# Performance work log

Measured on AMD Instinct MI355X. Metric: run time of the kernel, lower is better.

The kernel has to match this reference:

```python
import jax, jax.numpy as jnp
import numpy as np

B, T, I, H, O = 32, 128, 256, 512, 10


def setup_inputs() -> dict:
    key = jax.random.key(0)
    ks = jax.random.split(key, 16)
    s = 1.0 / np.sqrt(H)
    si = 1.0 / np.sqrt(I)
    inp = {
        "x": jax.random.normal(ks[0], (B, T, I), jnp.float32),
        # LSTM params (gate order: i, f, g, o)
        "Wih": jax.random.uniform(ks[1], (4 * H, I), jnp.float32, -si, si),
        "Whh": jax.random.uniform(ks[2], (4 * H, H), jnp.float32, -s, s),
        "b_lstm": jax.random.uniform(ks[3], (4 * H,), jnp.float32, -s, s),
        # readout dense
        "Wd": jax.random.uniform(ks[4], (O, H), jnp.float32, -s, s),
        "bd": jnp.zeros((O,), jnp.float32),
        # synthetic gradient MLP: H -> 512 -> 256 -> 128 -> H
        "Ws1": jax.random.uniform(ks[5], (512, H), jnp.float32, -s, s),
        "bs1": jnp.zeros((512,), jnp.float32),
        "Ws2": jax.random.uniform(ks[6], (256, 512), jnp.float32, -1.0 / np.sqrt(512), 1.0 / np.sqrt(512)),
        "bs2": jnp.zeros((256,), jnp.float32),
        "Ws3": jax.random.uniform(ks[7], (128, 256), jnp.float32, -1.0 / np.sqrt(256), 1.0 / np.sqrt(256)),
        "bs3": jnp.zeros((128,), jnp.float32),
        "Ws4": jax.random.uniform(ks[8], (H, 128), jnp.float32, -1.0 / np.sqrt(128), 1.0 / np.sqrt(128)),
        "bs4": jnp.zeros((H,), jnp.float32),
    }
    return inp


def reference(x, Wih, Whh, b_lstm, Wd, bd, Ws1, bs1, Ws2, bs2, Ws3, bs3, Ws4, bs4):
    # batch_first: [B,T,I] -> [T,B,I]
    xs = jnp.swapaxes(x, 0, 1)
    b, hid = x.shape[0], Whh.shape[1]

    h0 = jnp.zeros((b, hid), x.dtype)
    c0 = jnp.zeros((b, hid), x.dtype)
    # e-prop eligibility vectors: one row per (gate in {i,f,g}) x hidden unit
    ev_x0 = jnp.zeros((b, 3 * hid, Wih.shape[1]), x.dtype)
    ev_h0 = jnp.zeros((b, 3 * hid, hid), x.dtype)
    ev_b0 = jnp.zeros((b, 3 * hid, 1), x.dtype)

    def step(carry, xt):
        h, c, ev_x, ev_h, ev_b = carry
        gates = xt @ Wih.T + h @ Whh.T + b_lstm  # [B,4H]
        gi, gf, gg, go = jnp.split(gates, 4, axis=1)
        i = jax.nn.sigmoid(gi)
        f = jax.nn.sigmoid(gf)
        g = jnp.tanh(gg)
        o = jax.nn.sigmoid(go)
        # d(c_t)/d(pre-activation) for cell-affecting gates i, f, g  -> [B,3H]
        d = jnp.concatenate([g * i * (1.0 - i),
                             c * f * (1.0 - f),
                             i * (1.0 - g * g)], axis=1)
        f3 = jnp.concatenate([f, f, f], axis=1)  # forget-gate decay, tiled per gate
        # eligibility trace outer-product updates (the memory-bound core)
        ev_x_n = ev_x * f3[:, :, None] + d[:, :, None] * xt[:, None, :]
        ev_h_n = ev_h * f3[:, :, None] + d[:, :, None] * h[:, None, :]
        ev_b_n = ev_b * f3[:, :, None] + d[:, :, None]
        c_n = f * c + i * g
        h_n = o * jnp.tanh(c_n)
        return (h_n, c_n, ev_x_n, ev_h_n, ev_b_n), h_n

    (hT, cT, ev_x, ev_h, ev_b), hs = jax.lax.scan(step, (h0, c0, ev_x0, ev_h0, ev_b0), xs)

    last = hs[-1]  # [B,H]
    # synthetic gradient MLP on last hidden state
    z = jax.nn.relu(last @ Ws1.T + bs1)
    z = jax.nn.relu(z @ Ws2.T + bs2)
    z = jax.nn.relu(z @ Ws3.T + bs3)
    synth_grad = z @ Ws4.T + bs4  # [B,H]
    # readout on last hidden state (single_output=True)
    predictions = last @ Wd.T + bd  # [B,O]
    return (predictions, synth_grad, ev_x, ev_h, ev_b)
```

## Files before the change

kernel.cpp:

```cpp
#include <hip/hip_runtime.h>


typedef __attribute__((ext_vector_type(8))) short short8;
typedef __attribute__((ext_vector_type(4))) float f32x4;
typedef __attribute__((ext_vector_type(4))) unsigned u32x4;

#define DEV static __device__ __forceinline__

DEV unsigned f2bf(float x) {
  union { float f; unsigned u; } v; v.f = x;
  return (v.u + 0x7fffu + ((v.u >> 16) & 1u)) >> 16;
}
DEV float bf2f(unsigned b) {
  union { float f; unsigned u; } v; v.u = b << 16;
  return v.f;
}
struct HiLo { unsigned hi, lo; };
DEV HiLo packpair(float a, float b) {
  unsigned ha = f2bf(a), hb = f2bf(b);
  unsigned la = f2bf(a - bf2f(ha)), lb = f2bf(b - bf2f(hb));
  HiLo r; r.hi = ha | (hb << 16); r.lo = la | (lb << 16);
  return r;
}

__global__ __launch_bounds__(512, 1) void lstm_rec(
    const float* __restrict__ Whh,
    const float* __restrict__ XW,
    unsigned* __restrict__ Hp,
    float* __restrict__ Hf,
    float* __restrict__ dh,
    float* __restrict__ fh,
    unsigned* __restrict__ flags)
{
  const int wg   = blockIdx.x;
  const int tid  = threadIdx.x;
  const int lane = tid & 63;
  const int wave = tid >> 6;
  const int tM   = wave & 1;
  const int tN   = wave >> 1;

  __shared__ __align__(16) unsigned Ldh[32 * 256];
  __shared__ __align__(16) unsigned Ldl[32 * 256];
  __shared__ float gl[32][68];

  const int cc = lane & 15;
  const int kb = lane >> 4;

  const int rloc  = tN * 16 + cc;
  const int jglob = (rloc >> 4) * 512 + wg * 16 + (rloc & 15);
  short8 whi[16], wlo[16];
#pragma unroll
  for (int s = 0; s < 16; ++s) {
    const float* wp = Whh + (size_t)jglob * 512 + s * 32 + kb * 8;
    f32x4 w0 = *(const f32x4*)wp;
    f32x4 w1 = *(const f32x4*)(wp + 4);
    short8 hi, lo;
#pragma unroll
    for (int j = 0; j < 4; ++j) {
      unsigned h0 = f2bf(w0[j]);
      hi[j] = (short)h0;  lo[j] = (short)f2bf(w0[j] - bf2f(h0));
      unsigned h1 = f2bf(w1[j]);
      hi[4 + j] = (short)h1;  lo[4 + j] = (short)f2bf(w1[j] - bf2f(h1));
    }
    whi[s] = hi; wlo[s] = lo;
  }

  const int bA = tM * 16 + cc;
  const int mz = bA & 7;
  const unsigned rbase = (unsigned)(bA * 256 + ((kb ^ (mz & 3)) << 2) + ((mz >> 2) << 4));

  const int beW = lane >> 1;
  const int swz = beW & 7;

  const int be = tid >> 4;
  const int jo = tid & 15;
  const int jh = wg * 16 + jo;
  float c_reg = 0.f;

  for (int t = 0; t < 128; ++t) {
    const float* xwp = XW + (size_t)t * 65536 + (size_t)be * 2048 + wg * 16 + jo;
    float xwi = xwp[0], xwf = xwp[512], xwg = xwp[1024], xwo = xwp[1536];

    if (t > 0) {
      const unsigned long long* fl =
          (const unsigned long long*)(flags + t * 32 + wave * 4);
      for (;;) {
        unsigned long long f0 = __hip_atomic_load(fl, __ATOMIC_RELAXED,
                                                  __HIP_MEMORY_SCOPE_AGENT);
        unsigned long long f1 = __hip_atomic_load(fl + 1, __ATOMIC_RELAXED,
                                                  __HIP_MEMORY_SCOPE_AGENT);
        unsigned long long v = f0 & f1;
        if (v & (v >> 32) & 1ull) break;
        __builtin_amdgcn_s_sleep(1);
      }

      const unsigned* sp = Hp + ((size_t)t * 32 + wave * 4) * 512 + lane * 4;
      u32x4 h0, l0, h1, l1, h2, l2, h3, l3;
#define SLICE_LOAD(dst, addr)                                          \
      asm volatile("global_load_dwordx4 %0, %1, off sc0 sc1"           \
                   : "=&v"(dst) : "v"(addr) : "memory")
      SLICE_LOAD(h0, sp);
      SLICE_LOAD(l0, sp + 256);
      SLICE_LOAD(h1, sp + 512);
      SLICE_LOAD(l1, sp + 768);
      SLICE_LOAD(h2, sp + 1024);
      SLICE_LOAD(l2, sp + 1280);
      SLICE_LOAD(h3, sp + 1536);
      SLICE_LOAD(l3, sp + 1792);
#undef SLICE_LOAD
      asm volatile("s_waitcnt vmcnt(0)" ::: "memory");
      __builtin_amdgcn_sched_barrier(0);

      const int c0 = wave * 8 + (lane & 1);
      const unsigned wb = (unsigned)(beW * 256);
      *(u32x4*)&Ldh[wb + (((c0 + 0) ^ swz) << 2)] = h0;
      *(u32x4*)&Ldl[wb + (((c0 + 0) ^ swz) << 2)] = l0;
      *(u32x4*)&Ldh[wb + (((c0 + 2) ^ swz) << 2)] = h1;
      *(u32x4*)&Ldl[wb + (((c0 + 2) ^ swz) << 2)] = l1;
      *(u32x4*)&Ldh[wb + (((c0 + 4) ^ swz) << 2)] = h2;
      *(u32x4*)&Ldl[wb + (((c0 + 4) ^ swz) << 2)] = l2;
      *(u32x4*)&Ldh[wb + (((c0 + 6) ^ swz) << 2)] = h3;
      *(u32x4*)&Ldl[wb + (((c0 + 6) ^ swz) << 2)] = l3;
    }
    __syncthreads();

    f32x4 acc = {0.f, 0.f, 0.f, 0.f};
    if (t > 0) {
#pragma unroll
      for (int s = 0; s < 16; ++s) {
        const unsigned idx = rbase ^ (unsigned)(s << 4);
        short8 ah = __builtin_bit_cast(short8, *(const u32x4*)&Ldh[idx]);
        short8 al = __builtin_bit_cast(short8, *(const u32x4*)&Ldl[idx]);
        acc = __builtin_amdgcn_mfma_f32_16x16x32_bf16(ah, whi[s], acc, 0, 0, 0);
        acc = __builtin_amdgcn_mfma_f32_16x16x32_bf16(ah, wlo[s], acc, 0, 0, 0);
        acc = __builtin_amdgcn_mfma_f32_16x16x32_bf16(al, whi[s], acc, 0, 0, 0);
      }
    }
#pragma unroll
    for (int r = 0; r < 4; ++r)
      gl[tM * 16 + kb * 4 + r][tN * 16 + cc] = acc[r];
    __syncthreads();

    {
      float pi = xwi + gl[be][jo];
      float pf = xwf + gl[be][16 + jo];
      float pg = xwg + gl[be][32 + jo];
      float po = xwo + gl[be][48 + jo];
      float ig = 1.f / (1.f + expf(-pi));
      float fg = 1.f / (1.f + expf(-pf));
      float gg = tanhf(pg);
      float og = 1.f / (1.f + expf(-po));
      float di = gg * ig * (1.f - ig);
      float df = c_reg * fg * (1.f - fg);
      float dg = ig * (1.f - gg * gg);
      c_reg = fg * c_reg + ig * gg;
      float hn = og * tanhf(c_reg);
      Hf[(size_t)(t + 1) * 16384 + (size_t)be * 512 + jh] = hn;
      size_t db = (size_t)t * 49152 + (size_t)be * 1536 + jh;
      dh[db] = di; dh[db + 512] = df; dh[db + 1024] = dg;
      fh[(size_t)t * 16384 + (size_t)be * 512 + jh] = fg;

      unsigned hh = f2bf(hn);
      unsigned hl = f2bf(hn - bf2f(hh));
      unsigned hh_nb = (unsigned)__shfl_xor((int)hh, 1);
      unsigned hl_nb = (unsigned)__shfl_xor((int)hl, 1);
      size_t sb = ((size_t)(t + 1) * 32 + wg) * 512;
      unsigned stv; size_t sa;
      if (tid & 1) { stv = hl_nb | (hl << 16); sa = sb + 256 + (tid >> 1); }
      else         { stv = hh | (hh_nb << 16); sa = sb + (tid >> 1); }
      __hip_atomic_store(&Hp[sa], stv, __ATOMIC_RELAXED, __HIP_MEMORY_SCOPE_AGENT);
    }

    asm volatile("s_waitcnt vmcnt(0)" ::: "memory");
    __syncthreads();
    if (tid == 0)
      __hip_atomic_store(&flags[(t + 1) * 32 + wg], 1u,
                         __ATOMIC_RELAXED, __HIP_MEMORY_SCOPE_AGENT);
  }
}

__global__ __launch_bounds__(256) void suffix_pre(
    const float* __restrict__ fh, float* __restrict__ Cp)
{
  const int g = blockIdx.x * 256 + threadIdx.x;
  const int k = g >> 14, bjh = g & 16383;
  const int b = bjh >> 9, jh = bjh & 511;
  float P = 1.f;
  for (int t = k * 32; t < k * 32 + 32; ++t)
    P *= fh[(size_t)t * 16384 + (size_t)b * 512 + jh];
  Cp[g] = P;
}

__global__ __launch_bounds__(256) void suffix_main(
    float* __restrict__ dh, const float* __restrict__ fh,
    const float* __restrict__ Cp, float* __restrict__ Sp)
{
  const int g = blockIdx.x * 256 + threadIdx.x;
  const int k = g >> 14, bjh = g & 16383;
  const int b = bjh >> 9, jh = bjh & 511;
  float F = 1.f;
  for (int k2 = k + 1; k2 < 4; ++k2) F *= Cp[(k2 << 14) | bjh];
  float s0 = 0.f, s1 = 0.f, s2 = 0.f;
  for (int t = k * 32 + 31; t >= k * 32; --t) {
    size_t db = (size_t)t * 49152 + (size_t)b * 1536 + jh;
    float a0 = dh[db] * F, a1 = dh[db + 512] * F, a2 = dh[db + 1024] * F;
    dh[db] = a0; dh[db + 512] = a1; dh[db + 1024] = a2;
    s0 += a0; s1 += a1; s2 += a2;
    F *= fh[(size_t)t * 16384 + (size_t)b * 512 + jh];
  }
  size_t sb = (size_t)(k * 32 + b) * 1536 + jh;
  Sp[sb] = s0; Sp[sb + 512] = s1; Sp[sb + 1024] = s2;
}

__global__ __launch_bounds__(256) void evb_reduce(
    const float* __restrict__ Sp, float* __restrict__ evb)
{
  const int g = blockIdx.x * 256 + threadIdx.x;
  evb[g] = Sp[g] + Sp[49152 + g] + Sp[98304 + g] + Sp[147456 + g];
}

__global__ __launch_bounds__(256, 2) void gemm_bf16s(
    const float* __restrict__ A, const float* __restrict__ B,
    float* __restrict__ C, const float* __restrict__ bias,
    int M, int N, int K,
    long long sAm, long long sAk, long long aBatch,
    long long sBn, long long sBk, long long bBatch,
    long long sCm1, long long sCm2, int M1, long long cBatch)
{
  __shared__ __align__(16) unsigned Ahi[128 * 20], Alo[128 * 20];
  __shared__ __align__(16) unsigned Bhi[128 * 20], Blo[128 * 20];

  const int tid  = threadIdx.x;
  const int lane = tid & 63;
  const int wave = tid >> 6;
  const int wm   = wave >> 1;
  const int wn   = wave & 1;
  const int cc   = lane & 15;
  const int kb   = lane >> 4;
  const long long z = blockIdx.z;
  const float* Ab = A + z * aBatch;
  const float* Bb = B + z * bBatch;
  const int m0 = blockIdx.y * 128, n0 = blockIdx.x * 128;

  f32x4 acc[4][4];
#pragma unroll
  for (int i = 0; i < 4; ++i)
#pragma unroll
    for (int j = 0; j < 4; ++j) acc[i][j] = (f32x4){0.f, 0.f, 0.f, 0.f};

  for (int k0 = 0; k0 < K; k0 += 32) {
    if (sAk == 1) {
      const int r = tid >> 1, half = tid & 1;
      const float* s = Ab + (long long)(m0 + r) * sAm + (k0 + half * 16);
      f32x4 v0 = *(const f32x4*)s;
      f32x4 v1 = *(const f32x4*)(s + 4);
      f32x4 v2 = *(const f32x4*)(s + 8);
      f32x4 v3 = *(const f32x4*)(s + 12);
      u32x4 h0, h1, l0, l1;
      HiLo p;
      p = packpair(v0[0], v0[1]); h0[0] = p.hi; l0[0] = p.lo;
      p = packpair(v0[2], v0[3]); h0[1] = p.hi; l0[1] = p.lo;
      p = packpair(v1[0], v1[1]); h0[2] = p.hi; l0[2] = p.lo;
      p = packpair(v1[2], v1[3]); h0[3] = p.hi; l0[3] = p.lo;
      p = packpair(v2[0], v2[1]); h1[0] = p.hi; l1[0] = p.lo;
      p = packpair(v2[2], v2[3]); h1[1] = p.hi; l1[1] = p.lo;
      p = packpair(v3[0], v3[1]); h1[2] = p.hi; l1[2] = p.lo;
      p = packpair(v3[2], v3[3]); h1[3] = p.hi; l1[3] = p.lo;
      const int o = r * 20 + half * 8;
      *(u32x4*)&Ahi[o] = h0;  *(u32x4*)&Ahi[o + 4] = h1;
      *(u32x4*)&Alo[o] = l0;  *(u32x4*)&Alo[o + 4] = l1;
    } else {
#pragma unroll
      for (int it = 0; it < 2; ++it) {
        const int kp = tid >> 4;
        const int mr = (tid & 15) * 4 + it * 64;
        const float* s0 = Ab + (long long)(k0 + 2 * kp) * sAk + (m0 + mr);
        f32x4 va = *(const f32x4*)s0;
        f32x4 vb = *(const f32x4*)(s0 + sAk);
#pragma unroll
        for (int q = 0; q < 4; ++q) {
          HiLo p = packpair(va[q], vb[q]);
          Ahi[(mr + q) * 20 + kp] = p.hi;
          Alo[(mr + q) * 20 + kp] = p.lo;
        }
      }
    }
    if (sBk == 1) {
      const int r = tid >> 1, half = tid & 1;
      const float* s = Bb + (long long)(n0 + r) * sBn + (k0 + half * 16);
      f32x4 v0 = *(const f32x4*)s;
      f32x4 v1 = *(const f32x4*)(s + 4);
      f32x4 v2 = *(const f32x4*)(s + 8);
      f32x4 v3 = *(const f32x4*)(s + 12);
      u32x4 h0, h1, l0, l1;
      HiLo p;
      p = packpair(v0[0], v0[1]); h0[0] = p.hi; l0[0] = p.lo;
      p = packpair(v0[2], v0[3]); h0[1] = p.hi; l0[1] = p.lo;
      p = packpair(v1[0], v1[1]); h0[2] = p.hi; l0[2] = p.lo;
      p = packpair(v1[2], v1[3]); h0[3] = p.hi; l0[3] = p.lo;
      p = packpair(v2[0], v2[1]); h1[0] = p.hi; l1[0] = p.lo;
      p = packpair(v2[2], v2[3]); h1[1] = p.hi; l1[1] = p.lo;
      p = packpair(v3[0], v3[1]); h1[2] = p.hi; l1[2] = p.lo;
      p = packpair(v3[2], v3[3]); h1[3] = p.hi; l1[3] = p.lo;
      const int o = r * 20 + half * 8;
      *(u32x4*)&Bhi[o] = h0;  *(u32x4*)&Bhi[o + 4] = h1;
      *(u32x4*)&Blo[o] = l0;  *(u32x4*)&Blo[o + 4] = l1;
    } else {
#pragma unroll
      for (int it = 0; it < 2; ++it) {
        const int kp = tid >> 4;
        const int nr = (tid & 15) * 4 + it * 64;
        const float* s0 = Bb + (long long)(k0 + 2 * kp) * sBk + (n0 + nr);
        f32x4 va = *(const f32x4*)s0;
        f32x4 vb = *(const f32x4*)(s0 + sBk);
#pragma unroll
        for (int q = 0; q < 4; ++q) {
          HiLo p = packpair(va[q], vb[q]);
          Bhi[(nr + q) * 20 + kp] = p.hi;
          Blo[(nr + q) * 20 + kp] = p.lo;
        }
      }
    }
    __syncthreads();

    short8 ah[4], al[4], bh[4], bl[4];
#pragma unroll
    for (int mi = 0; mi < 4; ++mi) {
      const int row = wm * 64 + mi * 16 + cc;
      ah[mi] = __builtin_bit_cast(short8, *(const u32x4*)&Ahi[row * 20 + kb * 4]);
      al[mi] = __builtin_bit_cast(short8, *(const u32x4*)&Alo[row * 20 + kb * 4]);
    }
#pragma unroll
    for (int ni = 0; ni < 4; ++ni) {
      const int row = wn * 64 + ni * 16 + cc;
      bh[ni] = __builtin_bit_cast(short8, *(const u32x4*)&Bhi[row * 20 + kb * 4]);
      bl[ni] = __builtin_bit_cast(short8, *(const u32x4*)&Blo[row * 20 + kb * 4]);
    }
#pragma unroll
    for (int mi = 0; mi < 4; ++mi)
#pragma unroll
      for (int ni = 0; ni < 4; ++ni) {
        acc[mi][ni] = __builtin_amdgcn_mfma_f32_16x16x32_bf16(ah[mi], bh[ni], acc[mi][ni], 0, 0, 0);
        acc[mi][ni] = __builtin_amdgcn_mfma_f32_16x16x32_bf16(ah[mi], bl[ni], acc[mi][ni], 0, 0, 0);
        acc[mi][ni] = __builtin_amdgcn_mfma_f32_16x16x32_bf16(al[mi], bh[ni], acc[mi][ni], 0, 0, 0);
      }
    __syncthreads();
  }

#pragma unroll
  for (int ni = 0; ni < 4; ++ni) {
    const int ng = n0 + wn * 64 + ni * 16 + cc;
    const float bv = bias ? bias[ng] : 0.f;
#pragma unroll
    for (int mi = 0; mi < 4; ++mi) {
#pragma unroll
      for (int r = 0; r < 4; ++r) {
        const int mg = m0 + wm * 64 + mi * 16 + kb * 4 + r;
        const long long crow = z * cBatch + (long long)(mg % M1) * sCm1 +
                               (long long)(mg / M1) * sCm2;
        C[crow + ng] = acc[mi][ni][r] + bv;
      }
    }
  }
}

template <int BM, int BN, int TM, int TN>
__global__ __launch_bounds__(256) void gemm_f32(
    const float* __restrict__ A, const float* __restrict__ B,
    float* __restrict__ C, const float* __restrict__ bias,
    int M, int N, int K,
    long long sAm, long long sAk, long long aBatch,
    long long sBn, long long sBk, long long bBatch,
    long long sCm1, long long sCm2, int M1, long long cBatch,
    int relu)
{
  constexpr int BK = 16;
  __shared__ float As[BK][BM + 4];
  __shared__ float Bs[BK][BN + 4];
  const int tid = threadIdx.x;
  const long long z = blockIdx.z;
  const float* Ab = A + z * aBatch;
  const float* Bb = B + z * bBatch;
  const int m0 = blockIdx.y * BM, n0 = blockIdx.x * BN;
  constexpr int tn_cnt = BN / TN;
  const int tm0 = (tid / tn_cnt) * TM;
  const int tn0 = (tid % tn_cnt) * TN;

  float acc[TM][TN];
#pragma unroll
  for (int i = 0; i < TM; ++i)
#pragma unroll
    for (int j = 0; j < TN; ++j) acc[i][j] = 0.f;

  for (int k0 = 0; k0 < K; k0 += BK) {
    if (sAk == 1) {
      for (int m = tid >> 2; m < BM; m += 64) {
        const int kq = (tid & 3) * 4;
        f32x4 v = {0.f, 0.f, 0.f, 0.f};
        if (m0 + m < M) v = *(const f32x4*)(Ab + (long long)(m0 + m) * sAm + (k0 + kq));
        As[kq + 0][m] = v[0]; As[kq + 1][m] = v[1];
        As[kq + 2][m] = v[2]; As[kq + 3][m] = v[3];
      }
    } else {
      constexpr int mq_cnt = BM / 4;
      for (int kk = tid / mq_cnt; kk < BK; kk += 256 / mq_cnt) {
        const int mq = (tid % mq_cnt) * 4;
        f32x4 v = {0.f, 0.f, 0.f, 0.f};
        if (m0 + mq < M) v = *(const f32x4*)(Ab + (long long)(k0 + kk) * sAk + (m0 + mq));
        *(f32x4*)&As[kk][mq] = v;
      }
    }
    if (sBk == 1) {
      for (int n = tid >> 2; n < BN; n += 64) {
        const int kq = (tid & 3) * 4;
        f32x4 v = {0.f, 0.f, 0.f, 0.f};
        if (n0 + n < N) v = *(const f32x4*)(Bb + (long long)(n0 + n) * sBn + (k0 + kq));
        Bs[kq + 0][n] = v[0]; Bs[kq + 1][n] = v[1];
        Bs[kq + 2][n] = v[2]; Bs[kq + 3][n] = v[3];
      }
    } else {
      constexpr int nq_cnt = BN / 4;
      for (int kk = tid / nq_cnt; kk < BK; kk += 256 / nq_cnt) {
        const int nq = (tid % nq_cnt) * 4;
        f32x4 v = {0.f, 0.f, 0.f, 0.f};
        if (n0 + nq < N) v = *(const f32x4*)(Bb + (long long)(k0 + kk) * sBk + (n0 + nq));
        *(f32x4*)&Bs[kk][nq] = v;
      }
    }
    __syncthreads();

#pragma unroll
    for (int kk = 0; kk < BK; ++kk) {
      float a[TM], bb[TN];
#pragma unroll
      for (int i = 0; i < TM; ++i) a[i] = As[kk][tm0 + i];
#pragma unroll
      for (int j = 0; j < TN; ++j) bb[j] = Bs[kk][tn0 + j];
#pragma unroll
      for (int i = 0; i < TM; ++i)
#pragma unroll
        for (int j = 0; j < TN; ++j) acc[i][j] += a[i] * bb[j];
    }
    __syncthreads();
  }

#pragma unroll
  for (int i = 0; i < TM; ++i) {
    const int mg = m0 + tm0 + i;
    if (mg >= M) continue;
    const long long crow = z * cBatch + (long long)(mg % M1) * sCm1 +
                           (long long)(mg / M1) * sCm2;
#pragma unroll
    for (int j = 0; j < TN; ++j) {
      const int ng = n0 + tn0 + j;
      if (ng >= N) continue;
      float v = acc[i][j];
      if (bias) v += bias[ng];
      if (relu) v = fmaxf(v, 0.f);
      C[crow + ng] = v;
    }
  }
}

extern "C" void kernel_launch(void* const* d_in, const int* in_sizes, int n_in,
                              void* d_out, int out_size, void* d_ws, size_t ws_size,
                              hipStream_t stream) {
  const float* x   = (const float*)d_in[0];
  const float* Wih = (const float*)d_in[1];
  const float* Whh = (const float*)d_in[2];
  const float* bl  = (const float*)d_in[3];
  const float* Wd  = (const float*)d_in[4];
  const float* bd  = (const float*)d_in[5];
  const float* Ws1 = (const float*)d_in[6];
  const float* bs1 = (const float*)d_in[7];
  const float* Ws2 = (const float*)d_in[8];
  const float* bs2 = (const float*)d_in[9];
  const float* Ws3 = (const float*)d_in[10];
  const float* bs3 = (const float*)d_in[11];
  const float* Ws4 = (const float*)d_in[12];
  const float* bs4 = (const float*)d_in[13];

  float* out = (float*)d_out;
  float* ws  = (float*)d_ws;

  const long long OP = 0, OS = 320, OEX = 16704, OEH = 12599616, OEB = 37765440;

  float* XW = out + OEH;
  float* fh = out + OEH + 8388608;
  unsigned* Hp = (unsigned*)(out + OEH + 10485760);
  float* Cp = out + OEH + 12599296;
  float* Sp = out + OEH + 12664832;

  float* dh = ws;
  float* Hf = ws + 6291456;
  float* z1 = ws + 8404992;
  float* z2 = ws + 8421376;
  float* z3 = ws + 8429568;
  unsigned* flags = (unsigned*)(ws + 8433664);

  hipMemsetAsync(flags, 0, 129 * 32 * sizeof(unsigned), stream);
  hipMemsetAsync(Hf, 0, 16384 * sizeof(float), stream);

  dim3 blk(256);

  gemm_bf16s<<<dim3(16, 32, 1), blk, 0, stream>>>(
      x, Wih, XW, bl, 4096, 2048, 256,
      256, 1, 0,
      256, 1, 0,
      65536, 2048, 128, 0);

  lstm_rec<<<dim3(32), dim3(512), 0, stream>>>(Whh, XW, Hp, Hf, dh, fh, flags);

  suffix_pre<<<dim3(256), blk, 0, stream>>>(fh, Cp);
  suffix_main<<<dim3(256), blk, 0, stream>>>(dh, fh, Cp, Sp);
  evb_reduce<<<dim3(192), blk, 0, stream>>>(Sp, out + OEB);

  const float* hlast = Hf + 2097152;
  gemm_f32<32, 32, 2, 2><<<dim3(16, 1, 1), blk, 0, stream>>>(
      hlast, Ws1, z1, bs1, 32, 512, 512, 512, 1, 0, 512, 1, 0, 512, 0, 32, 0, 1);
  gemm_f32<32, 32, 2, 2><<<dim3(8, 1, 1), blk, 0, stream>>>(
      z1, Ws2, z2, bs2, 32, 256, 512, 512, 1, 0, 512, 1, 0, 256, 0, 32, 0, 1);
  gemm_f32<32, 32, 2, 2><<<dim3(4, 1, 1), blk, 0, stream>>>(
      z2, Ws3, z3, bs3, 32, 128, 256, 256, 1, 0, 256, 1, 0, 128, 0, 32, 0, 1);
  gemm_f32<32, 32, 2, 2><<<dim3(16, 1, 1), blk, 0, stream>>>(
      z3, Ws4, out + OS, bs4, 32, 512, 128, 128, 1, 0, 128, 1, 0, 512, 0, 32, 0, 0);
  gemm_f32<32, 32, 2, 2><<<dim3(1, 1, 1), blk, 0, stream>>>(
      hlast, Wd, out + OP, bd, 32, 10, 512, 512, 1, 0, 512, 1, 0, 10, 0, 32, 0, 0);

  gemm_bf16s<<<dim3(2, 12, 32), blk, 0, stream>>>(
      dh, x, out + OEX, nullptr, 1536, 256, 128,
      1, 49152, 1536,
      1, 256, 32768,
      256, 0, 1536, 393216);

  gemm_bf16s<<<dim3(4, 12, 32), blk, 0, stream>>>(
      dh, Hf, out + OEH, nullptr, 1536, 512, 128,
      1, 49152, 1536,
      1, 16384, 512,
      512, 0, 1536, 786432);
}
```

Baseline: 775.8 us.

## Replace flag handshake with sentinel-filled data polling in LSTM recurrence

Removes the per-step flag array and its release barrier. Each block now pre-fills the hidden-state exchange buffer with a sentinel pattern and spins on the data itself until no sentinel words remain, which cuts a store-wait-sync-flag round trip from the serial critical path. Side-output stores move after the h exchange store, and the three MFMA chains use independent accumulators to shorten the dependency chain. The scheme relies on the bf16-pair encoding never equalling 0x7F7F7F7F and on stores being visible without an explicit fence, and it adds a larger memset.

```diff
diff --git a/kernel.cpp b/kernel.cpp
--- a/kernel.cpp
+++ b/kernel.cpp
@@ -23,14 +23,15 @@
   return r;
 }
 
+#define SENT 0x7F7F7F7Fu
+
 __global__ __launch_bounds__(512, 1) void lstm_rec(
     const float* __restrict__ Whh,
     const float* __restrict__ XW,
     unsigned* __restrict__ Hp,
     float* __restrict__ Hf,
     float* __restrict__ dh,
-    float* __restrict__ fh,
-    unsigned* __restrict__ flags)
+    float* __restrict__ fh)
 {
   const int wg   = blockIdx.x;
   const int tid  = threadIdx.x;
@@ -82,33 +83,32 @@
     float xwi = xwp[0], xwf = xwp[512], xwg = xwp[1024], xwo = xwp[1536];
 
     if (t > 0) {
-      const unsigned long long* fl =
-          (const unsigned long long*)(flags + t * 32 + wave * 4);
-      for (;;) {
-        unsigned long long f0 = __hip_atomic_load(fl, __ATOMIC_RELAXED,
-                                                  __HIP_MEMORY_SCOPE_AGENT);
-        unsigned long long f1 = __hip_atomic_load(fl + 1, __ATOMIC_RELAXED,
-                                                  __HIP_MEMORY_SCOPE_AGENT);
-        unsigned long long v = f0 & f1;
-        if (v & (v >> 32) & 1ull) break;
-        __builtin_amdgcn_s_sleep(1);
-      }
-
       const unsigned* sp = Hp + ((size_t)t * 32 + wave * 4) * 512 + lane * 4;
       u32x4 h0, l0, h1, l1, h2, l2, h3, l3;
+      for (;;) {
 #define SLICE_LOAD(dst, addr)                                          \
-      asm volatile("global_load_dwordx4 %0, %1, off sc0 sc1"           \
-                   : "=&v"(dst) : "v"(addr) : "memory")
-      SLICE_LOAD(h0, sp);
-      SLICE_LOAD(l0, sp + 256);
-      SLICE_LOAD(h1, sp + 512);
-      SLICE_LOAD(l1, sp + 768);
-      SLICE_LOAD(h2, sp + 1024);
-      SLICE_LOAD(l2, sp + 1280);
-      SLICE_LOAD(h3, sp + 1536);
-      SLICE_LOAD(l3, sp + 1792);
+        asm volatile("global_load_dwordx4 %0, %1, off sc0 sc1"         \
+                     : "=&v"(dst) : "v"(addr) : "memory")
+        SLICE_LOAD(h0, sp);
+        SLICE_LOAD(l0, sp + 256);
+        SLICE_LOAD(h1, sp + 512);
+        SLICE_LOAD(l1, sp + 768);
+        SLICE_LOAD(h2, sp + 1024);
+        SLICE_LOAD(l2, sp + 1280);
+        SLICE_LOAD(h3, sp + 1536);
+        SLICE_LOAD(l3, sp + 1792);
 #undef SLICE_LOAD
-      asm volatile("s_waitcnt vmcnt(0)" ::: "memory");
+        asm volatile("s_waitcnt vmcnt(0)" ::: "memory");
+        __builtin_amdgcn_sched_barrier(0);
+        unsigned bad = 0u;
+#define CHK(v) bad |= (unsigned)((v[0] == SENT) | (v[1] == SENT) | \
+                                 (v[2] == SENT) | (v[3] == SENT))
+        CHK(h0); CHK(l0); CHK(h1); CHK(l1);
+        CHK(h2); CHK(l2); CHK(h3); CHK(l3);
+#undef CHK
+        if (!__any((int)bad)) break;
+        __builtin_amdgcn_s_sleep(1);
+      }
       __builtin_amdgcn_sched_barrier(0);
 
       const int c0 = wave * 8 + (lane & 1);
@@ -124,17 +124,21 @@
     }
     __syncthreads();
 
-    f32x4 acc = {0.f, 0.f, 0.f, 0.f};
-    if (t > 0) {
-#pragma unroll
-      for (int s = 0; s < 16; ++s) {
-        const unsigned idx = rbase ^ (unsigned)(s << 4);
-        short8 ah = __builtin_bit_cast(short8, *(const u32x4*)&Ldh[idx]);
-        short8 al = __builtin_bit_cast(short8, *(const u32x4*)&Ldl[idx]);
-        acc = __builtin_amdgcn_mfma_f32_16x16x32_bf16(ah, whi[s], acc, 0, 0, 0);
-        acc = __builtin_amdgcn_mfma_f32_16x16x32_bf16(ah, wlo[s], acc, 0, 0, 0);
-        acc = __builtin_amdgcn_mfma_f32_16x16x32_bf16(al, whi[s], acc, 0, 0, 0);
-      }
+    f32x4 acc;
+    {
+      f32x4 a0 = {0.f, 0.f, 0.f, 0.f}, a1 = a0, a2 = a0;
+      if (t > 0) {
+#pragma unroll
+        for (int s = 0; s < 16; ++s) {
+          const unsigned idx = rbase ^ (unsigned)(s << 4);
+          short8 ah = __builtin_bit_cast(short8, *(const u32x4*)&Ldh[idx]);
+          short8 al = __builtin_bit_cast(short8, *(const u32x4*)&Ldl[idx]);
+          a0 = __builtin_amdgcn_mfma_f32_16x16x32_bf16(ah, whi[s], a0, 0, 0, 0);
+          a1 = __builtin_amdgcn_mfma_f32_16x16x32_bf16(ah, wlo[s], a1, 0, 0, 0);
+          a2 = __builtin_amdgcn_mfma_f32_16x16x32_bf16(al, whi[s], a2, 0, 0, 0);
+        }
+      }
+      acc = a0 + (a1 + a2);
     }
 #pragma unroll
     for (int r = 0; r < 4; ++r)
@@ -155,10 +159,6 @@
       float dg = ig * (1.f - gg * gg);
       c_reg = fg * c_reg + ig * gg;
       float hn = og * tanhf(c_reg);
-      Hf[(size_t)(t + 1) * 16384 + (size_t)be * 512 + jh] = hn;
-      size_t db = (size_t)t * 49152 + (size_t)be * 1536 + jh;
-      dh[db] = di; dh[db + 512] = df; dh[db + 1024] = dg;
-      fh[(size_t)t * 16384 + (size_t)be * 512 + jh] = fg;
 
       unsigned hh = f2bf(hn);
       unsigned hl = f2bf(hn - bf2f(hh));
@@ -169,13 +169,12 @@
       if (tid & 1) { stv = hl_nb | (hl << 16); sa = sb + 256 + (tid >> 1); }
       else         { stv = hh | (hh_nb << 16); sa = sb + (tid >> 1); }
       __hip_atomic_store(&Hp[sa], stv, __ATOMIC_RELAXED, __HIP_MEMORY_SCOPE_AGENT);
-    }
-
-    asm volatile("s_waitcnt vmcnt(0)" ::: "memory");
-    __syncthreads();
-    if (tid == 0)
-      __hip_atomic_store(&flags[(t + 1) * 32 + wg], 1u,
-                         __ATOMIC_RELAXED, __HIP_MEMORY_SCOPE_AGENT);
+
+      Hf[(size_t)(t + 1) * 16384 + (size_t)be * 512 + jh] = hn;
+      size_t db = (size_t)t * 49152 + (size_t)be * 1536 + jh;
+      dh[db] = di; dh[db + 512] = df; dh[db + 1024] = dg;
+      fh[(size_t)t * 16384 + (size_t)be * 512 + jh] = fg;
+    }
   }
 }
 
@@ -496,9 +495,8 @@
   float* z1 = ws + 8404992;
   float* z2 = ws + 8421376;
   float* z3 = ws + 8429568;
-  unsigned* flags = (unsigned*)(ws + 8433664);
-
-  hipMemsetAsync(flags, 0, 129 * 32 * sizeof(unsigned), stream);
+
+  hipMemsetAsync(Hp, 0x7F, 129ull * 32 * 512 * sizeof(unsigned), stream);
   hipMemsetAsync(Hf, 0, 16384 * sizeof(float), stream);
 
   dim3 blk(256);
@@ -509,7 +507,7 @@
       256, 1, 0,
       65536, 2048, 128, 0);
 
-  lstm_rec<<<dim3(32), dim3(512), 0, stream>>>(Whh, XW, Hp, Hf, dh, fh, flags);
+  lstm_rec<<<dim3(32), dim3(512), 0, stream>>>(Whh, XW, Hp, Hf, dh, fh);
 
   suffix_pre<<<dim3(256), blk, 0, stream>>>(fh, Cp);
   suffix_main<<<dim3(256), blk, 0, stream>>>(dh, fh, Cp, Sp);
```

New measurement: 774.4 us. About the same (-0.2%).
